# Kernel optimization log

Measured on AMD Instinct MI355X. Metric: run time of the kernel, lower is better.

Reference implementation:

```python
import jax, jax.numpy as jnp
import numpy as np

# dims: B=4 batch, S=512 seq, P=128 input_size, C=64 classes(=hidden_size), K=64 gln layer width, 4 context bits -> 16 contexts
B, S, P, C, K, NBITS = 4, 512, 128, 64, 64, 4
NCTX = 2 ** NBITS
LOGIT_CLIP = 5.0


def setup_inputs() -> dict:
    key = jax.random.key(0)
    ks = jax.random.split(key, 8)
    return {
        "x": jax.random.normal(ks[0], (B, S, P), jnp.float32),
        "hidden": jax.random.normal(ks[1], (B, C), jnp.float32),
        # GLN layer 1: per-class, per-neuron halfspace context hyperplanes and gated weights
        "H1": jax.random.normal(ks[2], (C, K, NBITS, P), jnp.float32),
        "W1": jax.random.normal(ks[3], (C, K, NCTX, P), jnp.float32) / np.sqrt(P),
        # GLN output layer: one neuron per class
        "H2": jax.random.normal(ks[4], (C, NBITS, P), jnp.float32),
        "W2": jax.random.normal(ks[5], (C, NCTX, K), jnp.float32) / np.sqrt(K),
        # fc2: Linear(input_size, hidden_size)
        "fc2_w": jax.random.normal(ks[6], (C, P), jnp.float32) / np.sqrt(P),
        "fc2_b": jnp.zeros((C,), jnp.float32),
    }


def _ctx_index(bits):
    # bits: (..., NBITS) bool -> integer context id in [0, 2^NBITS)
    return (bits * (2 ** jnp.arange(NBITS, dtype=jnp.int32))).sum(-1)


def _gln_predict(x, H1, W1, H2, W2):
    # base predictions: sigmoid(x) -> logit space is x itself (clipped for stability)
    l0 = jnp.clip(x, -LOGIT_CLIP, LOGIT_CLIP)  # (B,S,P)
    # layer 1: halfspace gating then geometric mixing in logit space
    ctx1 = _ctx_index(jnp.einsum('bsp,ckjp->bsckj', x, H1) > 0)          # (B,S,C,K)
    mix1 = jnp.einsum('bsp,ckxp->bsckx', l0, W1)                          # (B,S,C,K,NCTX)
    l1 = jnp.take_along_axis(mix1, ctx1[..., None], axis=-1)[..., 0]      # (B,S,C,K)
    l1 = jnp.clip(l1, -LOGIT_CLIP, LOGIT_CLIP)
    # output layer: one gated neuron per class
    ctx2 = _ctx_index(jnp.einsum('bsp,cjp->bscj', x, H2) > 0)             # (B,S,C)
    mix2 = jnp.einsum('bsck,cxk->bscx', l1, W2)                           # (B,S,C,NCTX)
    l2 = jnp.take_along_axis(mix2, ctx2[..., None], axis=-1)[..., 0]      # (B,S,C)
    return jax.nn.sigmoid(l2)


def reference(x, hidden, H1, W1, H2, W2, fc2_w, fc2_b):
    b = _gln_predict(x, H1, W1, H2, W2)                   # (B,S,C)
    # multihead gating
    sig_alphas = jax.nn.sigmoid(x @ fc2_w.T + fc2_b)      # (B,S,C)
    b = b * sig_alphas

    # sequential roll+add+relu recurrence over seq_len
    def step(h, bt):
        h = jax.nn.relu(bt + jnp.roll(h, 1, axis=-1))
        return h, h

    h_last, outs = jax.lax.scan(step, hidden, jnp.swapaxes(b, 0, 1))  # outs: (S,B,C)
    outputs = jnp.swapaxes(outs, 0, 1)                                # (B,S,C)
    return outputs, h_last
```

## Files before the change

### kernel.cpp

```cpp
#include <hip/hip_runtime.h>
#include <math.h>

#define BB 4
#define SS 512
#define PP 128
#define CC 64
#define KK 64
#define NCTX_ 16
#define TT 64
#define NTILES ((BB*SS)/TT)

typedef __attribute__((ext_vector_type(8))) short bf16x8;
typedef __attribute__((ext_vector_type(4))) float f32x4;
typedef __attribute__((ext_vector_type(16))) float f32x16;

static __device__ __forceinline__ float bf2f(short h) {
    unsigned u = ((unsigned)(unsigned short)h) << 16;
    return __builtin_bit_cast(float, u);
}
static __device__ __forceinline__ short f2bf(float f) {
    unsigned u = __builtin_bit_cast(unsigned, f);
    unsigned r = (u + 0x7fffu + ((u >> 16) & 1u)) >> 16;
    return (short)(unsigned short)r;
}
static __device__ __forceinline__ bf16x8 clampfrag(bf16x8 h) {
    typedef __attribute__((ext_vector_type(4))) unsigned u32x4;
    u32x4 u = __builtin_bit_cast(u32x4, h);
    #pragma unroll
    for (int i = 0; i < 4; ++i) {
        const unsigned w = u[i];
        const unsigned s = w & 0x80008000u;
        unsigned lo = w & 0x7fffu;
        unsigned hi = (w >> 16) & 0x7fffu;
        lo = lo > 0x40a0u ? 0x40a0u : lo;
        hi = hi > 0x40a0u ? 0x40a0u : hi;
        u[i] = s | lo | (hi << 16);
    }
    return __builtin_bit_cast(bf16x8, u);
}

__global__ __launch_bounds__(256) void pack_kernel(
    const float* __restrict__ W1, const float* __restrict__ H1,
    const float* __restrict__ H2, const float* __restrict__ fc2w,
    short* __restrict__ W1h, short* __restrict__ H1h32, short* __restrict__ H1l32,
    short* __restrict__ H2Wh, short* __restrict__ H2Wl)
{
    const int bid  = blockIdx.x;
    const int w    = threadIdx.x >> 6;
    const int lane = threadIdx.x & 63;

    if (bid < CC * KK) {
        const int tile = bid;
        const int q    = w;
        const float4* src = reinterpret_cast<const float4*>(
            W1 + ((size_t)tile * 16 + (lane >> 2)) * PP + q * 32 + (lane & 3) * 8);
        const float4 v0 = src[0], v1 = src[1];
        const float vv[8] = {v0.x, v0.y, v0.z, v0.w, v1.x, v1.y, v1.z, v1.w};
        bf16x8 hh;
        #pragma unroll
        for (int e = 0; e < 8; ++e) hh[e] = f2bf(vv[e]);
        const int lp = (lane & 3) * 16 + (lane >> 2);
        *reinterpret_cast<bf16x8*>(W1h + (((size_t)tile * 4 + q) * 64 + lp) * 8) = hh;
    } else if (bid < CC * KK + 1024) {
        const int gw  = (bid - CC * KK) * 4 + w;
        const int row = (gw >> 3) * 32 + (lane & 31);
        const int col = (gw & 7) * 16 + (lane >> 5) * 8;
        const float4* s = reinterpret_cast<const float4*>(H1 + (size_t)row * PP + col);
        const float4 a = s[0], b = s[1];
        const float vv[8] = {a.x, a.y, a.z, a.w, b.x, b.y, b.z, b.w};
        bf16x8 hh, ll;
        #pragma unroll
        for (int e = 0; e < 8; ++e) {
            const short hv = f2bf(vv[e]);
            hh[e] = hv;
            ll[e] = f2bf(vv[e] - bf2f(hv));
        }
        const size_t o = ((size_t)gw * 64 + lane) * 8;
        *reinterpret_cast<bf16x8*>(H1h32 + o) = hh;
        *reinterpret_cast<bf16x8*>(H1l32 + o) = ll;
    } else {
        const int cidx = bid - (CC * KK + 1024);
        #pragma unroll
        for (int i = 0; i < 2; ++i) {
            const int q8  = w * 2 + i;
            const int row = lane & 31;
            const int col = q8 * 16 + (lane >> 5) * 8;
            float vv[8];
            if (row < 4) {
                const float4* s = reinterpret_cast<const float4*>(
                    H2 + ((size_t)cidx * 4 + row) * PP + col);
                const float4 a = s[0], b = s[1];
                vv[0]=a.x; vv[1]=a.y; vv[2]=a.z; vv[3]=a.w;
                vv[4]=b.x; vv[5]=b.y; vv[6]=b.z; vv[7]=b.w;
            } else if (row == 4) {
                const float4* s = reinterpret_cast<const float4*>(
                    fc2w + (size_t)cidx * PP + col);
                const float4 a = s[0], b = s[1];
                vv[0]=a.x; vv[1]=a.y; vv[2]=a.z; vv[3]=a.w;
                vv[4]=b.x; vv[5]=b.y; vv[6]=b.z; vv[7]=b.w;
            } else {
                #pragma unroll
                for (int e = 0; e < 8; ++e) vv[e] = 0.f;
            }
            bf16x8 hh, ll;
            #pragma unroll
            for (int e = 0; e < 8; ++e) {
                const short hv = f2bf(vv[e]);
                hh[e] = hv;
                ll[e] = f2bf(vv[e] - bf2f(hv));
            }
            const size_t o = (((size_t)cidx * 8 + q8) * 64 + lane) * 8;
            *reinterpret_cast<bf16x8*>(H2Wh + o) = hh;
            *reinterpret_cast<bf16x8*>(H2Wl + o) = ll;
        }
    }
}

__global__ __launch_bounds__(256, 4) void predict_kernel(
    const float* __restrict__ x,
    const short* __restrict__ H1h32,
    const short* __restrict__ H1l32,
    const short* __restrict__ W1h,
    const short* __restrict__ H2Wh,
    const short* __restrict__ H2Wl,
    const float* __restrict__ W2,
    const float* __restrict__ fc2b,
    float* __restrict__ bout)
{
    __shared__ short xuh[2][8][64][8];
    __shared__ unsigned char ctxb[TT][68];
    __shared__ unsigned char bit2b[TT];
    __shared__ float af[TT];

    const int tid  = threadIdx.x;
    const int lane = tid & 63;
    const int wid  = __builtin_amdgcn_readfirstlane(tid >> 6);
    const int bid  = blockIdx.x;
    const int sw   = ((bid & 7) << 8) | (bid >> 3);
    const int c    = sw >> 5;
    const int tile = sw & (NTILES - 1);
    const int tok0 = tile * TT;

    const int t15 = lane & 15;
    const int g   = lane >> 4;
    const int l31 = lane & 31;
    const int l5  = lane >> 5;
    const unsigned laneo = (unsigned)lane * 8u;
    const f32x4  zero4  = {0.f, 0.f, 0.f, 0.f};
    const f32x16 zero16 = {0.f,0.f,0.f,0.f,0.f,0.f,0.f,0.f,
                           0.f,0.f,0.f,0.f,0.f,0.f,0.f,0.f};

    {
        const int tok = tid >> 2;
        const int qq  = tid & 3;
        const int ct  = tok >> 5;
        const float4* x4 = reinterpret_cast<const float4*>(
            x + (size_t)(tok0 + tok) * PP + qq * 32);
        float v[32];
        #pragma unroll
        for (int i = 0; i < 8; ++i) {
            const float4 t = x4[i];
            v[i*4+0]=t.x; v[i*4+1]=t.y; v[i*4+2]=t.z; v[i*4+3]=t.w;
        }
        #pragma unroll
        for (int gg = 0; gg < 4; ++gg) {
            const int q8 = qq * 2 + (gg >> 1);
            const int lw = (gg & 1) * 32 + (tok & 31);
            bf16x8 hh;
            #pragma unroll
            for (int e = 0; e < 8; ++e) hh[e] = f2bf(v[gg*8+e]);
            *reinterpret_cast<bf16x8*>(&xuh[ct][q8][lw][0]) = hh;
        }
    }
    __syncthreads();

    #pragma unroll
    for (int rt = 0; rt < 2; ++rt) {
        f32x16 aA = zero16, aB = zero16;
        const short* hb = H1h32 + (unsigned)((c * 8 + wid * 2 + rt) * 8) * 512u;
        const short* lb = H1l32 + (unsigned)((c * 8 + wid * 2 + rt) * 8) * 512u;
        #pragma unroll
        for (int q8 = 0; q8 < 8; ++q8) {
            const unsigned off = (unsigned)(q8 * 512) + laneo;
            const bf16x8 ah  = *reinterpret_cast<const bf16x8*>(hb + off);
            const bf16x8 al  = *reinterpret_cast<const bf16x8*>(lb + off);
            const bf16x8 bh0 = *reinterpret_cast<const bf16x8*>(&xuh[0][q8][lane][0]);
            const bf16x8 bh1 = *reinterpret_cast<const bf16x8*>(&xuh[1][q8][lane][0]);
            aA = __builtin_amdgcn_mfma_f32_32x32x16_bf16(ah, bh0, aA, 0, 0, 0);
            aA = __builtin_amdgcn_mfma_f32_32x32x16_bf16(al, bh0, aA, 0, 0, 0);
            aB = __builtin_amdgcn_mfma_f32_32x32x16_bf16(ah, bh1, aB, 0, 0, 0);
            aB = __builtin_amdgcn_mfma_f32_32x32x16_bf16(al, bh1, aB, 0, 0, 0);
        }
        #pragma unroll
        for (int rg = 0; rg < 4; ++rg) {
            const int k = wid * 16 + rt * 8 + 2 * rg + l5;
            const int cvA = (aA[4*rg+0] > 0.f ? 1 : 0) | (aA[4*rg+1] > 0.f ? 2 : 0) |
                            (aA[4*rg+2] > 0.f ? 4 : 0) | (aA[4*rg+3] > 0.f ? 8 : 0);
            const int cvB = (aB[4*rg+0] > 0.f ? 1 : 0) | (aB[4*rg+1] > 0.f ? 2 : 0) |
                            (aB[4*rg+2] > 0.f ? 4 : 0) | (aB[4*rg+3] > 0.f ? 8 : 0);
            ctxb[l31][k]      = (unsigned char)cvA;
            ctxb[32 + l31][k] = (unsigned char)cvB;
        }
    }

    if (wid < 2) {
        f32x16 a2 = zero16;
        const short* hb = H2Wh + (unsigned)(c * 8) * 512u;
        const short* lb = H2Wl + (unsigned)(c * 8) * 512u;
        #pragma unroll
        for (int q8 = 0; q8 < 8; ++q8) {
            const unsigned off = (unsigned)(q8 * 512) + laneo;
            const bf16x8 ah = *reinterpret_cast<const bf16x8*>(hb + off);
            const bf16x8 al = *reinterpret_cast<const bf16x8*>(lb + off);
            const bf16x8 bh = *reinterpret_cast<const bf16x8*>(&xuh[wid][q8][lane][0]);
            a2 = __builtin_amdgcn_mfma_f32_32x32x16_bf16(ah, bh, a2, 0, 0, 0);
            a2 = __builtin_amdgcn_mfma_f32_32x32x16_bf16(al, bh, a2, 0, 0, 0);
        }
        const int tok = wid * 32 + l31;
        if (l5 == 0) {
            bit2b[tok] = (unsigned char)((a2[0] > 0.f ? 1 : 0) | (a2[1] > 0.f ? 2 : 0) |
                                         (a2[2] > 0.f ? 4 : 0) | (a2[3] > 0.f ? 8 : 0));
        } else {
            af[tok] = a2[0];
        }
    }

    short* l1s = &xuh[0][0][0][0];
    {
        bf16x8 ch[4][4];
        #pragma unroll
        for (int j = 0; j < 4; ++j)
            #pragma unroll
            for (int q = 0; q < 4; ++q) {
                const int q8 = 2 * q + (g >> 1);
                const int lw = (g & 1) * 32 + (j & 1) * 16 + t15;
                ch[j][q] = clampfrag(*reinterpret_cast<const bf16x8*>(&xuh[j >> 1][q8][lw][0]));
            }
        __syncthreads();

        const short* wb = W1h + (unsigned)((c * KK + wid * 16) * 4) * 512u;
        #pragma unroll 4
        for (int k16 = 0; k16 < 16; ++k16) {
            const int k = wid * 16 + k16;
            const unsigned ko = (unsigned)(k16 * 2048) + laneo;
            f32x4 acc[4] = {zero4, zero4, zero4, zero4};
            #pragma unroll
            for (int q = 0; q < 4; ++q) {
                const bf16x8 ah = *reinterpret_cast<const bf16x8*>(wb + ko + (unsigned)(q * 512));
                #pragma unroll
                for (int j = 0; j < 4; ++j)
                    acc[j] = __builtin_amdgcn_mfma_f32_16x16x32_bf16(ah, ch[j][q], acc[j], 0, 0, 0);
            }
            #pragma unroll
            for (int j = 0; j < 4; ++j) {
                const int tok = j * 16 + t15;
                const int cx  = ctxb[tok][k];
                const int sel = cx & 3;
                const float v = (sel == 0) ? acc[j][0] : (sel == 1) ? acc[j][1] :
                                (sel == 2) ? acc[j][2] : acc[j][3];
                if (g == (cx >> 2))
                    l1s[tok * 68 + k] = f2bf(fminf(fmaxf(v, -5.f), 5.f));
            }
        }
    }
    __syncthreads();

    {
        const int tok = tid >> 2;
        const int qt  = tid & 3;
        const int ctx2 = bit2b[tok];
        const float* w2p = W2 + (unsigned)((c * NCTX_ + ctx2) * KK + qt * 16);
        float s = 0.f;
        #pragma unroll
        for (int i4 = 0; i4 < 4; ++i4) {
            const float4 w = *reinterpret_cast<const float4*>(w2p + i4 * 4);
            const int kb = tok * 68 + qt * 16 + i4 * 4;
            s = fmaf(w.x, bf2f(l1s[kb + 0]),
                fmaf(w.y, bf2f(l1s[kb + 1]),
                fmaf(w.z, bf2f(l1s[kb + 2]),
                fmaf(w.w, bf2f(l1s[kb + 3]), s))));
        }
        s += __shfl_xor(s, 1, 64);
        s += __shfl_xor(s, 2, 64);
        if (qt == 0) {
            const float alpha = af[tok] + fc2b[c];
            const float bv = (1.f / (1.f + expf(-s))) * (1.f / (1.f + expf(-alpha)));
            bout[(unsigned)((tok0 + tok) * CC + c)] = bv;
        }
    }
}

__global__ __launch_bounds__(256, 4) void predict_fb_kernel(
    const float* __restrict__ x,
    const float* __restrict__ H1,
    const float* __restrict__ W1b,
    const float* __restrict__ H2,
    const float* __restrict__ W2,
    const float* __restrict__ fc2w,
    const float* __restrict__ fc2b,
    float* __restrict__ bout)
{
    __shared__ float xs[PP][TT + 1];
    __shared__ float bitss[4][TT];
    __shared__ float apart[4][TT];
    __shared__ float l2part[4][TT];

    const int tid  = threadIdx.x;
    const int lane = tid & 63;
    const int wid  = __builtin_amdgcn_readfirstlane(tid >> 6);
    const int bid  = blockIdx.x;
    const int sw   = ((bid & 7) << 8) | (bid >> 3);
    const int c    = sw >> 5;
    const int tile = sw & (NTILES - 1);
    const int tok0 = tile * TT;

    {
        const float4* xg = reinterpret_cast<const float4*>(x + (size_t)tok0 * PP);
        #pragma unroll
        for (int it = 0; it < (TT * PP / 4) / 256; ++it) {
            const int i = it * 256 + tid;
            const float4 v = xg[i];
            const int t = i >> 5;
            const int p = (i & 31) << 2;
            xs[p + 0][t] = v.x; xs[p + 1][t] = v.y;
            xs[p + 2][t] = v.z; xs[p + 3][t] = v.w;
        }
    }
    __syncthreads();

    int ctxreg[16];
    {
        const float4* H1c4 = reinterpret_cast<const float4*>(H1 + (size_t)c * KK * 4 * PP);
        #pragma unroll
        for (int gg = 0; gg < 8; ++gg) {
            const int k = wid * 16 + gg * 2;
            const float4* h4 = H1c4 + (size_t)k * 4 * 32;
            float acc[8] = {0.f, 0.f, 0.f, 0.f, 0.f, 0.f, 0.f, 0.f};
            #pragma unroll 2
            for (int p4 = 0; p4 < 32; ++p4) {
                const float x0 = xs[4 * p4 + 0][lane];
                const float x1 = xs[4 * p4 + 1][lane];
                const float x2 = xs[4 * p4 + 2][lane];
                const float x3 = xs[4 * p4 + 3][lane];
                #pragma unroll
                for (int r = 0; r < 8; ++r) {
                    const float4 w = h4[r * 32 + p4];
                    acc[r] = fmaf(w.w, x3, fmaf(w.z, x2, fmaf(w.y, x1, fmaf(w.x, x0, acc[r]))));
                }
            }
            ctxreg[gg * 2]     = (acc[0] > 0.f ? 1 : 0) | (acc[1] > 0.f ? 2 : 0) |
                                 (acc[2] > 0.f ? 4 : 0) | (acc[3] > 0.f ? 8 : 0);
            ctxreg[gg * 2 + 1] = (acc[4] > 0.f ? 1 : 0) | (acc[5] > 0.f ? 2 : 0) |
                                 (acc[6] > 0.f ? 4 : 0) | (acc[7] > 0.f ? 8 : 0);
        }
    }
    {
        const float4* h2 = reinterpret_cast<const float4*>(H2 + ((size_t)c * 4 + wid) * PP);
        float d = 0.f;
        #pragma unroll 8
        for (int p4 = 0; p4 < 32; ++p4) {
            const float4 w = h2[p4];
            d = fmaf(w.w, xs[4 * p4 + 3][lane], fmaf(w.z, xs[4 * p4 + 2][lane],
                fmaf(w.y, xs[4 * p4 + 1][lane], fmaf(w.x, xs[4 * p4 + 0][lane], d))));
        }
        bitss[wid][lane] = (d > 0.f) ? 1.f : 0.f;
        const float4* fw = reinterpret_cast<const float4*>(fc2w + (size_t)c * PP) + wid * 8;
        float ap = 0.f;
        #pragma unroll
        for (int p4 = 0; p4 < 8; ++p4) {
            const float4 w = fw[p4];
            const int p = wid * 32 + 4 * p4;
            ap = fmaf(w.w, xs[p + 3][lane], fmaf(w.z, xs[p + 2][lane],
                 fmaf(w.y, xs[p + 1][lane], fmaf(w.x, xs[p + 0][lane], ap))));
        }
        apart[wid][lane] = ap;
    }
    __syncthreads();

    float l1v[16];
    {
        const float4* W1c4 = reinterpret_cast<const float4*>(W1b) +
                             (size_t)(c * KK + wid * 16) * 512;
        #pragma unroll
        for (int gg = 0; gg < 2; ++gg) {
            float s[8] = {0.f, 0.f, 0.f, 0.f, 0.f, 0.f, 0.f, 0.f};
            const float4* wp[8];
            #pragma unroll
            for (int jj = 0; jj < 8; ++jj) {
                const int kk = gg * 8 + jj;
                wp[jj] = W1c4 + (size_t)kk * 512 + (size_t)ctxreg[kk] * 32;
            }
            #pragma unroll 2
            for (int p4 = 0; p4 < 32; ++p4) {
                const float x0 = fminf(fmaxf(xs[4 * p4 + 0][lane], -5.f), 5.f);
                const float x1 = fminf(fmaxf(xs[4 * p4 + 1][lane], -5.f), 5.f);
                const float x2 = fminf(fmaxf(xs[4 * p4 + 2][lane], -5.f), 5.f);
                const float x3 = fminf(fmaxf(xs[4 * p4 + 3][lane], -5.f), 5.f);
                #pragma unroll
                for (int jj = 0; jj < 8; ++jj) {
                    const float4 wv = wp[jj][p4];
                    s[jj] = fmaf(wv.w, x3, fmaf(wv.z, x2, fmaf(wv.y, x1, fmaf(wv.x, x0, s[jj]))));
                }
            }
            #pragma unroll
            for (int jj = 0; jj < 8; ++jj)
                l1v[gg * 8 + jj] = fminf(fmaxf(s[jj], -5.f), 5.f);
        }
    }
    {
        const int ctx2 = (bitss[0][lane] > 0.5f ? 1 : 0) | (bitss[1][lane] > 0.5f ? 2 : 0) |
                         (bitss[2][lane] > 0.5f ? 4 : 0) | (bitss[3][lane] > 0.5f ? 8 : 0);
        const float* w2 = W2 + ((size_t)c * NCTX_ + ctx2) * KK + wid * 16;
        float lp = 0.f;
        #pragma unroll
        for (int jj = 0; jj < 16; ++jj) lp = fmaf(w2[jj], l1v[jj], lp);
        l2part[wid][lane] = lp;
    }
    __syncthreads();
    if (wid == 0) {
        const int t = lane;
        const float l2 = (l2part[0][t] + l2part[1][t]) + (l2part[2][t] + l2part[3][t]);
        const float alpha = apart[0][t] + apart[1][t] + apart[2][t] + apart[3][t] + fc2b[c];
        const float bv = (1.f / (1.f + expf(-l2))) * (1.f / (1.f + expf(-alpha)));
        bout[(size_t)(tok0 + t) * CC + c] = bv;
    }
}

__global__ __launch_bounds__(64) void scan_kernel(const float* __restrict__ hidden,
                                                  float* __restrict__ out)
{
    const int b    = blockIdx.x;
    const int lane = threadIdx.x;
    float* row = out + (size_t)b * SS * CC;
    const float hprev = hidden[b * CC + ((lane + 63) & 63)];

    float nb[64];
    #pragma unroll
    for (int j = 0; j < 64; ++j) nb[j] = row[j * CC + ((lane + j) & 63)];
    float acc = fmaxf(nb[0] + hprev, 0.f);
    row[lane] = acc;
    #pragma unroll
    for (int j = 1; j < 64; ++j) {
        acc += nb[j];
        row[j * CC + ((lane + j) & 63)] = acc;
    }
    for (int c0 = 64; c0 < SS; c0 += 64) {
        #pragma unroll
        for (int j = 0; j < 64; ++j)
            nb[j] = row[(c0 + j) * CC + ((lane + c0 + j) & 63)];
        #pragma unroll
        for (int j = 0; j < 64; ++j) {
            acc += nb[j];
            row[(c0 + j) * CC + ((lane + c0 + j) & 63)] = acc;
        }
    }
    out[(size_t)BB * SS * CC + b * CC + ((lane + 63) & 63)] = acc;
}

extern "C" void kernel_launch(void* const* d_in, const int* in_sizes, int n_in,
                              void* d_out, int out_size, void* d_ws, size_t ws_size,
                              hipStream_t stream) {
    const float* x      = (const float*)d_in[0];
    const float* hidden = (const float*)d_in[1];
    const float* H1     = (const float*)d_in[2];
    const float* W1     = (const float*)d_in[3];
    const float* H2     = (const float*)d_in[4];
    const float* W2     = (const float*)d_in[5];
    const float* fc2w   = (const float*)d_in[6];
    const float* fc2b   = (const float*)d_in[7];
    float* out = (float*)d_out;

    const size_t MB = 1024 * 1024;

    if (ws_size >= 25 * MB) {
        short* W1hp  = (short*)d_ws;
        short* H1hp  = (short*)((char*)d_ws + 16 * MB);
        short* H1lp  = (short*)((char*)d_ws + 20 * MB);
        short* H2Whp = (short*)((char*)d_ws + 24 * MB);
        short* H2Wlp = (short*)((char*)d_ws + 24 * MB + 512 * 1024);
        pack_kernel<<<dim3(CC * KK + 1024 + CC), 256, 0, stream>>>(
            W1, H1, H2, fc2w, W1hp, H1hp, H1lp, H2Whp, H2Wlp);
        predict_kernel<<<dim3(CC * NTILES), 256, 0, stream>>>(
            x, H1hp, H1lp, W1hp, H2Whp, H2Wlp, W2, fc2b, out);
    } else {
        predict_fb_kernel<<<dim3(CC * NTILES), 256, 0, stream>>>(
            x, H1, W1, H2, W2, fc2w, fc2b, out);
    }
    scan_kernel<<<dim3(BB), 64, 0, stream>>>(hidden, out);
}
```

Measured before the change: 98.74 us.

## Pre-pack x to bf16 fragments once and preload context bytes into registers

The pack kernel now also converts x into bf16 in the MFMA fragment layout. Previously each of the 64 class blocks per tile re-read fp32 x and re-converted it. predict_kernel now does a plain 16-byte copy of the packed tile into LDS. Context bytes for each wave's 16 neurons are preloaded as packed words before the barrier, and the k16 loop is fully unrolled. The cost is an extra 1 MB of workspace, which raises the workspace threshold, plus possible register pressure from the full unroll.

```diff
diff --git a/kernel.cpp b/kernel.cpp
--- a/kernel.cpp
+++ b/kernel.cpp
@@ -42,8 +42,10 @@
 __global__ __launch_bounds__(256) void pack_kernel(
     const float* __restrict__ W1, const float* __restrict__ H1,
     const float* __restrict__ H2, const float* __restrict__ fc2w,
+    const float* __restrict__ x,
     short* __restrict__ W1h, short* __restrict__ H1h32, short* __restrict__ H1l32,
-    short* __restrict__ H2Wh, short* __restrict__ H2Wl)
+    short* __restrict__ H2Wh, short* __restrict__ H2Wl,
+    short* __restrict__ xpk)
 {
     const int bid  = blockIdx.x;
     const int w    = threadIdx.x >> 6;
@@ -78,7 +80,7 @@
         const size_t o = ((size_t)gw * 64 + lane) * 8;
         *reinterpret_cast<bf16x8*>(H1h32 + o) = hh;
         *reinterpret_cast<bf16x8*>(H1l32 + o) = ll;
-    } else {
+    } else if (bid < CC * KK + 1024 + CC) {
         const int cidx = bid - (CC * KK + 1024);
         #pragma unroll
         for (int i = 0; i < 2; ++i) {
@@ -113,11 +115,25 @@
             *reinterpret_cast<bf16x8*>(H2Wh + o) = hh;
             *reinterpret_cast<bf16x8*>(H2Wl + o) = ll;
         }
+    } else {
+        const int frag = (bid - (CC * KK + 1024 + CC)) * 4 + w;
+        const int tile = frag >> 4;
+        const int ct   = (frag >> 3) & 1;
+        const int q8   = frag & 7;
+        const int row  = tile * 64 + ct * 32 + (lane & 31);
+        const int col  = q8 * 16 + (lane >> 5) * 8;
+        const float4* s = reinterpret_cast<const float4*>(x + (size_t)row * PP + col);
+        const float4 a = s[0], b = s[1];
+        const float vv[8] = {a.x, a.y, a.z, a.w, b.x, b.y, b.z, b.w};
+        bf16x8 hh;
+        #pragma unroll
+        for (int e = 0; e < 8; ++e) hh[e] = f2bf(vv[e]);
+        *reinterpret_cast<bf16x8*>(xpk + ((size_t)frag * 64 + lane) * 8) = hh;
     }
 }
 
 __global__ __launch_bounds__(256, 4) void predict_kernel(
-    const float* __restrict__ x,
+    const short* __restrict__ xpk,
     const short* __restrict__ H1h32,
     const short* __restrict__ H1l32,
     const short* __restrict__ W1h,
@@ -151,25 +167,12 @@
                            0.f,0.f,0.f,0.f,0.f,0.f,0.f,0.f};
 
     {
-        const int tok = tid >> 2;
-        const int qq  = tid & 3;
-        const int ct  = tok >> 5;
-        const float4* x4 = reinterpret_cast<const float4*>(
-            x + (size_t)(tok0 + tok) * PP + qq * 32);
-        float v[32];
-        #pragma unroll
-        for (int i = 0; i < 8; ++i) {
-            const float4 t = x4[i];
-            v[i*4+0]=t.x; v[i*4+1]=t.y; v[i*4+2]=t.z; v[i*4+3]=t.w;
-        }
-        #pragma unroll
-        for (int gg = 0; gg < 4; ++gg) {
-            const int q8 = qq * 2 + (gg >> 1);
-            const int lw = (gg & 1) * 32 + (tok & 31);
-            bf16x8 hh;
-            #pragma unroll
-            for (int e = 0; e < 8; ++e) hh[e] = f2bf(v[gg*8+e]);
-            *reinterpret_cast<bf16x8*>(&xuh[ct][q8][lw][0]) = hh;
+        const bf16x8* src = reinterpret_cast<const bf16x8*>(xpk) + (unsigned)tile * 1024u;
+        bf16x8* dst = reinterpret_cast<bf16x8*>(&xuh[0][0][0][0]);
+        #pragma unroll
+        for (int i = 0; i < 4; ++i) {
+            const int idx = i * 256 + tid;
+            dst[idx] = src[idx];
         }
     }
     __syncthreads();
@@ -236,10 +239,18 @@
                 const int lw = (g & 1) * 32 + (j & 1) * 16 + t15;
                 ch[j][q] = clampfrag(*reinterpret_cast<const bf16x8*>(&xuh[j >> 1][q8][lw][0]));
             }
+        unsigned cxw[4][4];
+        #pragma unroll
+        for (int j = 0; j < 4; ++j) {
+            const int tok = j * 16 + t15;
+            #pragma unroll
+            for (int i = 0; i < 4; ++i)
+                cxw[j][i] = *reinterpret_cast<const unsigned*>(&ctxb[tok][wid * 16 + i * 4]);
+        }
         __syncthreads();
 
         const short* wb = W1h + (unsigned)((c * KK + wid * 16) * 4) * 512u;
-        #pragma unroll 4
+        #pragma unroll
         for (int k16 = 0; k16 < 16; ++k16) {
             const int k = wid * 16 + k16;
             const unsigned ko = (unsigned)(k16 * 2048) + laneo;
@@ -254,7 +265,7 @@
             #pragma unroll
             for (int j = 0; j < 4; ++j) {
                 const int tok = j * 16 + t15;
-                const int cx  = ctxb[tok][k];
+                const int cx  = (int)((cxw[j][k16 >> 2] >> ((k16 & 3) * 8)) & 15u);
                 const int sel = cx & 3;
                 const float v = (sel == 0) ? acc[j][0] : (sel == 1) ? acc[j][1] :
                                 (sel == 2) ? acc[j][2] : acc[j][3];
@@ -472,16 +483,17 @@
 
     const size_t MB = 1024 * 1024;
 
-    if (ws_size >= 25 * MB) {
+    if (ws_size >= 26 * MB) {
         short* W1hp  = (short*)d_ws;
         short* H1hp  = (short*)((char*)d_ws + 16 * MB);
         short* H1lp  = (short*)((char*)d_ws + 20 * MB);
         short* H2Whp = (short*)((char*)d_ws + 24 * MB);
         short* H2Wlp = (short*)((char*)d_ws + 24 * MB + 512 * 1024);
-        pack_kernel<<<dim3(CC * KK + 1024 + CC), 256, 0, stream>>>(
-            W1, H1, H2, fc2w, W1hp, H1hp, H1lp, H2Whp, H2Wlp);
+        short* xpkp  = (short*)((char*)d_ws + 25 * MB);
+        pack_kernel<<<dim3(CC * KK + 1024 + CC + 128), 256, 0, stream>>>(
+            W1, H1, H2, fc2w, x, W1hp, H1hp, H1lp, H2Whp, H2Wlp, xpkp);
         predict_kernel<<<dim3(CC * NTILES), 256, 0, stream>>>(
-            x, H1hp, H1lp, W1hp, H2Whp, H2Wlp, W2, fc2b, out);
+            xpkp, H1hp, H1lp, W1hp, H2Whp, H2Wlp, W2, fc2b, out);
     } else {
         predict_fb_kernel<<<dim3(CC * NTILES), 256, 0, stream>>>(
             x, H1, W1, H2, W2, fc2w, fc2b, out);
```

After: 94.70 us. 4.1% less time.
